# Kernel optimization log

Measured on AMD Instinct MI355X. Metric: run time of the kernel, lower is better.

Reference implementation:

```python
import jax, jax.numpy as jnp
import numpy as np

N = 100000
E = 3200000
IN_DIM, HID_DIM, OUT_DIM = 29, 64, 2


def setup_inputs() -> dict:
    key = jax.random.key(0)
    k1, k2, k3, k4, k5 = jax.random.split(key, 5)
    x = jax.random.normal(k1, (N, IN_DIM), dtype=jnp.float32)
    edge_index = jax.random.randint(k2, (2, E), 0, N, dtype=jnp.int64)
    # GCNConv params: glorot-ish weights, zero bias (bias added after aggregation)
    W1 = jax.random.normal(k3, (IN_DIM, HID_DIM), dtype=jnp.float32) * (1.0 / np.sqrt(IN_DIM))
    b1 = jnp.zeros((HID_DIM,), dtype=jnp.float32)
    W2 = jax.random.normal(k4, (HID_DIM, OUT_DIM), dtype=jnp.float32) * (1.0 / np.sqrt(HID_DIM))
    b2 = jnp.zeros((OUT_DIM,), dtype=jnp.float32)
    return {"x": x, "edge_index": edge_index, "W1": W1, "b1": b1, "W2": W2, "b2": b2}


def _gcn_norm(edge_index, n_nodes):
    # PyG gcn_norm with add_self_loops=True, symmetric D^-1/2 A D^-1/2
    loop = jnp.arange(n_nodes, dtype=edge_index.dtype)
    src = jnp.concatenate([edge_index[0], loop])
    dst = jnp.concatenate([edge_index[1], loop])
    deg = jax.ops.segment_sum(jnp.ones_like(dst, dtype=jnp.float32), dst, num_segments=n_nodes)
    dinv = jnp.where(deg > 0, jax.lax.rsqrt(deg), 0.0)
    norm = dinv[src] * dinv[dst]  # [E + N]
    return src, dst, norm


def _gcn_conv(x, src, dst, norm, W, b):
    h = x @ W                      # [N, d_out] -- transform first (smaller msgs)
    msg = h[src] * norm[:, None]   # [E+N, d_out] gather + scale
    out = jax.ops.segment_sum(msg, dst, num_segments=x.shape[0])  # scatter-add
    return out + b


def reference(x, edge_index, W1, b1, W2, b2):
    src, dst, norm = _gcn_norm(edge_index, x.shape[0])
    h = _gcn_conv(x, src, dst, norm, W1, b1)
    h = jax.nn.relu(h)
    out = _gcn_conv(h, src, dst, norm, W2, b2)
    return out
```

## Files before the change

kernel.cpp:

```cpp
#include <hip/hip_runtime.h>

#define N_NODES 100000
#define N_EDGES 3200000
#define IN_DIM  29
#define HID_DIM 64
#define NBUCK   782
#define BNODES  128
#define CAP     5120
#define EPT     8
#define EPB     4096

#define OFF_CUR   0
#define OFF_ROWS  1024
#define OFF_ROWE  101024
#define OFF_DINV  201024
#define OFF_ZS    301024
#define OFF_EBUF  501024
#define OFF_XS    4504864

static __device__ __forceinline__ unsigned short f2bf(float f) {
    unsigned u = __float_as_uint(f);
    u += 0x7fffu + ((u >> 16) & 1u);
    return (unsigned short)(u >> 16);
}

static __device__ __forceinline__ void unpack_add(float4& acc, uint2 a) {
    acc.x += __uint_as_float(a.x << 16);
    acc.y += __uint_as_float(a.x & 0xFFFF0000u);
    acc.z += __uint_as_float(a.y << 16);
    acc.w += __uint_as_float(a.y & 0xFFFF0000u);
}

__global__ __launch_bounds__(512) void partition_kernel(const int* __restrict__ ei,
        int* __restrict__ gcursor, int* __restrict__ ebuf) {
    __shared__ int lhist[NBUCK];
    __shared__ int lcur[NBUCK];
    int tid = threadIdx.x;
    for (int i = tid; i < NBUCK; i += 512) lhist[i] = 0;
    __syncthreads();

    int base = blockIdx.x * EPB + tid * EPT;
    int dv[EPT], sv[EPT];
    bool valid = (base < N_EDGES);
    if (valid) {
        const int4* dp = (const int4*)(ei + N_EDGES + base);
        const int4* sp = (const int4*)(ei + base);
        #pragma unroll
        for (int q = 0; q < 2; ++q) {
            int4 t = dp[q];
            dv[4*q+0] = t.x; dv[4*q+1] = t.y; dv[4*q+2] = t.z; dv[4*q+3] = t.w;
            int4 u = sp[q];
            sv[4*q+0] = u.x; sv[4*q+1] = u.y; sv[4*q+2] = u.z; sv[4*q+3] = u.w;
        }
        #pragma unroll
        for (int j = 0; j < EPT; ++j) atomicAdd(&lhist[dv[j] >> 7], 1);
    }
    __syncthreads();
    for (int i = tid; i < NBUCK; i += 512) {
        int c = lhist[i];
        lcur[i] = c ? (atomicAdd(&gcursor[i], c) + i * CAP) : 0;
    }
    __syncthreads();
    if (valid) {
        #pragma unroll
        for (int j = 0; j < EPT; ++j) {
            int d = dv[j];
            int pos = atomicAdd(&lcur[d >> 7], 1);
            ebuf[pos] = sv[j] | ((d & 127) << 17);
        }
    }
}

__global__ __launch_bounds__(512) void bucketsort_kernel(const int* __restrict__ gcursor,
        int* __restrict__ ebuf, int* __restrict__ rowStart, int* __restrict__ rowEnd,
        float* __restrict__ dinv, const float* __restrict__ x,
        unsigned int* __restrict__ xsb) {
    __shared__ int   cnt[BNODES];
    __shared__ int   cur[BNODES];
    __shared__ float dls[BNODES];
    __shared__ int   stage[CAP];
    int b = blockIdx.x, tid = threadIdx.x;
    if (tid < BNODES) cnt[tid] = 0;
    __syncthreads();
    int base = b * CAP;
    int size = gcursor[b];

    for (int j = tid; j < size; j += 512)
        atomicAdd(&cnt[((unsigned)ebuf[base + j]) >> 17], 1);
    __syncthreads();

    if (tid < 64) {
        int a = cnt[2 * tid], bb = cnt[2 * tid + 1];
        int s = a + bb;
        int incl = s;
        #pragma unroll
        for (int off = 1; off < 64; off <<= 1) {
            int t = __shfl_up(incl, off);
            if ((int)tid >= off) incl += t;
        }
        int excl = incl - s;
        cur[2 * tid]     = excl;
        cur[2 * tid + 1] = excl + a;
    }
    __syncthreads();

    if (tid < BNODES) {
        int v = cnt[tid];
        int excl = cur[tid];
        int node = b * BNODES + tid;
        if (node < N_NODES) {
            rowStart[node] = base + excl;
            rowEnd[node]   = base + excl + v;
            float dn = rsqrtf((float)v + 1.0f);
            dinv[node] = dn;
            dls[tid] = dn;
        }
    }
    __syncthreads();

    for (int j = tid; j < size; j += 512) {
        unsigned p = (unsigned)ebuf[base + j];
        int pos = atomicAdd(&cur[p >> 17], 1);
        stage[pos] = p & 0x1FFFF;
    }
    __syncthreads();
    for (int j = tid; j < size; j += 512)
        ebuf[base + j] = stage[j];

    for (int i = tid; i < BNODES * 16; i += 512) {
        int dl = i >> 4, kp = i & 15;
        int nd = b * BNODES + dl;
        if (nd < N_NODES) {
            float dn = dls[dl];
            int k0 = kp * 2, k1 = k0 + 1;
            float f0 = (k0 < IN_DIM) ? x[nd * IN_DIM + k0] * dn : 0.0f;
            float f1 = (k1 < IN_DIM) ? x[nd * IN_DIM + k1] * dn : 0.0f;
            unsigned u = (unsigned)f2bf(f0) | ((unsigned)f2bf(f1) << 16);
            xsb[(size_t)nd * 16 + kp] = u;
        }
    }
}

__global__ __launch_bounds__(256) void fused_kernel(const unsigned int* __restrict__ xs_,
        const int* __restrict__ rowStart, const int* __restrict__ rowEnd,
        const int* __restrict__ ebuf, const float* __restrict__ dinv,
        const float* __restrict__ W1, const float* __restrict__ b1,
        const float* __restrict__ W2, float* __restrict__ zs) {
    __shared__ float w1s[IN_DIM * HID_DIM];
    __shared__ float b1s[HID_DIM];
    __shared__ float w2s[HID_DIM * 2];
    int tid = threadIdx.x;
    for (int i = tid; i < IN_DIM * HID_DIM; i += 256) w1s[i] = W1[i];
    if (tid < HID_DIM) {
        b1s[tid] = b1[tid];
        w2s[tid * 2 + 0] = W2[tid * 2 + 0];
        w2s[tid * 2 + 1] = W2[tid * 2 + 1];
    }
    __syncthreads();

    int lane = tid & 63;
    int q = lane >> 3, m = lane & 7;
    const uint2* xsb = (const uint2*)xs_;
    int nodeBase = blockIdx.x * 16 + (tid >> 6) * 4;

    for (int rep = 0; rep < 4; ++rep) {
        int node = nodeBase + rep;
        if (node >= N_NODES) break;

        float4 acc = make_float4(0.f, 0.f, 0.f, 0.f);
        if (q == 0)
            unpack_add(acc, xsb[(size_t)node * 8 + m]);

        int rs = rowStart[node], re = rowEnd[node];
        int last = re - 1;
        for (int j = rs + q; j < re; j += 32) {
            int j1 = j + 8, j2 = j + 16, j3 = j + 24;
            int s0 = ebuf[j];
            int s1 = ebuf[min(j1, last)];
            int s2 = ebuf[min(j2, last)];
            int s3 = ebuf[min(j3, last)];
            uint2 a  = xsb[(size_t)s0 * 8 + m];
            uint2 bb = xsb[(size_t)s1 * 8 + m];
            uint2 c  = xsb[(size_t)s2 * 8 + m];
            uint2 d  = xsb[(size_t)s3 * 8 + m];
            unpack_add(acc, a);
            if (j1 < re) unpack_add(acc, bb);
            if (j2 < re) unpack_add(acc, c);
            if (j3 < re) unpack_add(acc, d);
        }
        #pragma unroll
        for (int msk = 8; msk <= 32; msk <<= 1) {
            acc.x += __shfl_xor(acc.x, msk);
            acc.y += __shfl_xor(acc.y, msk);
            acc.z += __shfl_xor(acc.z, msk);
            acc.w += __shfl_xor(acc.w, msk);
        }
        float dn = dinv[node];
        acc.x *= dn; acc.y *= dn; acc.z *= dn; acc.w *= dn;

        float h = b1s[lane];
        #pragma unroll
        for (int kk = 0; kk < IN_DIM; ++kk) {
            float comp = ((kk & 3) == 0) ? acc.x : ((kk & 3) == 1) ? acc.y
                       : ((kk & 3) == 2) ? acc.z : acc.w;
            h = fmaf(__shfl(comp, kk >> 2), w1s[kk * HID_DIM + lane], h);
        }
        h = fmaxf(h, 0.0f);

        float z0 = h * w2s[lane * 2 + 0];
        float z1 = h * w2s[lane * 2 + 1];
        #pragma unroll
        for (int off = 32; off > 0; off >>= 1) {
            z0 += __shfl_down(z0, off);
            z1 += __shfl_down(z1, off);
        }
        if (lane == 0) {
            zs[node * 2 + 0] = z0 * dn;
            zs[node * 2 + 1] = z1 * dn;
        }
    }
}

__global__ __launch_bounds__(256) void agg2_kernel(const float* __restrict__ zs,
        const int* __restrict__ rowStart, const int* __restrict__ rowEnd,
        const int* __restrict__ ebuf, const float* __restrict__ dinv,
        const float* __restrict__ b2, float* __restrict__ out) {
    int tid = threadIdx.x;
    int node = blockIdx.x * 16 + (tid >> 4);
    if (node >= N_NODES) return;
    int gl = tid & 15;
    const float2* zs2 = (const float2*)zs;
    float a0 = 0.0f, a1 = 0.0f, c0 = 0.0f, c1 = 0.0f;
    int rs = rowStart[node], re = rowEnd[node];
    int last = re - 1;
    for (int j = rs + gl; j < re; j += 32) {
        int j1 = j + 16;
        float2 za = zs2[ebuf[j]];
        float2 zb = zs2[ebuf[min(j1, last)]];
        a0 += za.x; a1 += za.y;
        if (j1 < re) { c0 += zb.x; c1 += zb.y; }
    }
    a0 += c0; a1 += c1;
    a0 += __shfl_xor(a0, 8); a1 += __shfl_xor(a1, 8);
    a0 += __shfl_xor(a0, 4); a1 += __shfl_xor(a1, 4);
    a0 += __shfl_xor(a0, 2); a1 += __shfl_xor(a1, 2);
    a0 += __shfl_xor(a0, 1); a1 += __shfl_xor(a1, 1);
    if (gl == 0) {
        float dn = dinv[node];
        float2 zself = zs2[node];
        float2 o;
        o.x = dn * (a0 + zself.x) + b2[0];
        o.y = dn * (a1 + zself.y) + b2[1];
        ((float2*)out)[node] = o;
    }
}

extern "C" void kernel_launch(void* const* d_in, const int* in_sizes, int n_in,
                              void* d_out, int out_size, void* d_ws, size_t ws_size,
                              hipStream_t stream) {
    const float* x  = (const float*)d_in[0];
    const int*   ei = (const int*)d_in[1];
    const float* W1 = (const float*)d_in[2];
    const float* b1 = (const float*)d_in[3];
    const float* W2 = (const float*)d_in[4];
    const float* b2 = (const float*)d_in[5];
    float* out = (float*)d_out;

    int*   wsi      = (int*)d_ws;
    float* wsf      = (float*)d_ws;
    int*   gcursor  = wsi + OFF_CUR;
    int*   rowStart = wsi + OFF_ROWS;
    int*   rowEnd   = wsi + OFF_ROWE;
    float* dinv     = wsf + OFF_DINV;
    float* zs       = wsf + OFF_ZS;
    int*   ebuf     = wsi + OFF_EBUF;
    unsigned int* xsb = (unsigned int*)(wsi + OFF_XS);

    hipMemsetAsync(gcursor, 0, NBUCK * sizeof(int), stream);
    partition_kernel<<<(N_EDGES + EPB - 1) / EPB, 512, 0, stream>>>(ei, gcursor, ebuf);
    bucketsort_kernel<<<NBUCK, 512, 0, stream>>>(gcursor, ebuf, rowStart, rowEnd, dinv, x, xsb);
    fused_kernel<<<(N_NODES + 15) / 16, 256, 0, stream>>>(xsb, rowStart, rowEnd, ebuf, dinv, W1, b1, W2, zs);
    agg2_kernel<<<(N_NODES + 15) / 16, 256, 0, stream>>>(zs, rowStart, rowEnd, ebuf, dinv, b2, out);
}
```

Before: 229.3 us.

## Split bucket sort into degree count and fuse sort into layer-1 aggregation

Result: slower. 237.9 us (+3.8%).

```diff
diff --git a/kernel.cpp b/kernel.cpp
--- a/kernel.cpp
+++ b/kernel.cpp
@@ -4,19 +4,22 @@
 #define N_EDGES 3200000
 #define IN_DIM  29
 #define HID_DIM 64
-#define NBUCK   782
-#define BNODES  128
-#define CAP     5120
-#define EPT     8
-#define EPB     4096
+#define NBUCK   1563
+#define BNODES  64
+#define CAP     2560
+#define EPT     32
+#define EPB     16384
 
 #define OFF_CUR   0
-#define OFF_ROWS  1024
-#define OFF_ROWE  101024
-#define OFF_DINV  201024
-#define OFF_ZS    301024
-#define OFF_EBUF  501024
-#define OFF_XS    4504864
+#define OFF_DEGC  2048
+#define OFF_DINV  102080
+#define OFF_ROWS  202112
+#define OFF_ROWE  302144
+#define OFF_ZS    402176
+#define OFF_EBUF  602240
+#define OFF_XS    4603520
+
+typedef unsigned uv2 __attribute__((ext_vector_type(2)));
 
 static __device__ __forceinline__ unsigned short f2bf(float f) {
     unsigned u = __float_as_uint(f);
@@ -24,7 +27,7 @@
     return (unsigned short)(u >> 16);
 }
 
-static __device__ __forceinline__ void unpack_add(float4& acc, uint2 a) {
+static __device__ __forceinline__ void unpack_add(float4& acc, uv2 a) {
     acc.x += __uint_as_float(a.x << 16);
     acc.y += __uint_as_float(a.x & 0xFFFF0000u);
     acc.z += __uint_as_float(a.y << 16);
@@ -46,14 +49,14 @@
         const int4* dp = (const int4*)(ei + N_EDGES + base);
         const int4* sp = (const int4*)(ei + base);
         #pragma unroll
-        for (int q = 0; q < 2; ++q) {
+        for (int q = 0; q < 8; ++q) {
             int4 t = dp[q];
             dv[4*q+0] = t.x; dv[4*q+1] = t.y; dv[4*q+2] = t.z; dv[4*q+3] = t.w;
             int4 u = sp[q];
             sv[4*q+0] = u.x; sv[4*q+1] = u.y; sv[4*q+2] = u.z; sv[4*q+3] = u.w;
         }
         #pragma unroll
-        for (int j = 0; j < EPT; ++j) atomicAdd(&lhist[dv[j] >> 7], 1);
+        for (int j = 0; j < EPT; ++j) atomicAdd(&lhist[dv[j] >> 6], 1);
     }
     __syncthreads();
     for (int i = tid; i < NBUCK; i += 512) {
@@ -65,69 +68,37 @@
         #pragma unroll
         for (int j = 0; j < EPT; ++j) {
             int d = dv[j];
-            int pos = atomicAdd(&lcur[d >> 7], 1);
-            ebuf[pos] = sv[j] | ((d & 127) << 17);
-        }
-    }
-}
-
-__global__ __launch_bounds__(512) void bucketsort_kernel(const int* __restrict__ gcursor,
-        int* __restrict__ ebuf, int* __restrict__ rowStart, int* __restrict__ rowEnd,
-        float* __restrict__ dinv, const float* __restrict__ x,
+            int pos = atomicAdd(&lcur[d >> 6], 1);
+            ebuf[pos] = sv[j] | ((d & 63) << 17);
+        }
+    }
+}
+
+__global__ __launch_bounds__(256) void degcnt_kernel(const int* __restrict__ gcursor,
+        const int* __restrict__ ebuf, const float* __restrict__ x,
+        int* __restrict__ degc, float* __restrict__ dinv,
         unsigned int* __restrict__ xsb) {
     __shared__ int   cnt[BNODES];
-    __shared__ int   cur[BNODES];
     __shared__ float dls[BNODES];
-    __shared__ int   stage[CAP];
     int b = blockIdx.x, tid = threadIdx.x;
     if (tid < BNODES) cnt[tid] = 0;
     __syncthreads();
-    int base = b * CAP;
-    int size = gcursor[b];
-
-    for (int j = tid; j < size; j += 512)
+    int base = b * CAP, sz = gcursor[b];
+    for (int j = tid; j < sz; j += 256)
         atomicAdd(&cnt[((unsigned)ebuf[base + j]) >> 17], 1);
     __syncthreads();
-
-    if (tid < 64) {
-        int a = cnt[2 * tid], bb = cnt[2 * tid + 1];
-        int s = a + bb;
-        int incl = s;
-        #pragma unroll
-        for (int off = 1; off < 64; off <<= 1) {
-            int t = __shfl_up(incl, off);
-            if ((int)tid >= off) incl += t;
-        }
-        int excl = incl - s;
-        cur[2 * tid]     = excl;
-        cur[2 * tid + 1] = excl + a;
-    }
-    __syncthreads();
-
     if (tid < BNODES) {
-        int v = cnt[tid];
-        int excl = cur[tid];
         int node = b * BNODES + tid;
         if (node < N_NODES) {
-            rowStart[node] = base + excl;
-            rowEnd[node]   = base + excl + v;
-            float dn = rsqrtf((float)v + 1.0f);
+            int c = cnt[tid];
+            degc[node] = c;
+            float dn = rsqrtf((float)c + 1.0f);
             dinv[node] = dn;
             dls[tid] = dn;
         }
     }
     __syncthreads();
-
-    for (int j = tid; j < size; j += 512) {
-        unsigned p = (unsigned)ebuf[base + j];
-        int pos = atomicAdd(&cur[p >> 17], 1);
-        stage[pos] = p & 0x1FFFF;
-    }
-    __syncthreads();
-    for (int j = tid; j < size; j += 512)
-        ebuf[base + j] = stage[j];
-
-    for (int i = tid; i < BNODES * 16; i += 512) {
+    for (int i = tid; i < BNODES * 16; i += 256) {
         int dl = i >> 4, kp = i & 15;
         int nd = b * BNODES + dl;
         if (nd < N_NODES) {
@@ -135,58 +106,91 @@
             int k0 = kp * 2, k1 = k0 + 1;
             float f0 = (k0 < IN_DIM) ? x[nd * IN_DIM + k0] * dn : 0.0f;
             float f1 = (k1 < IN_DIM) ? x[nd * IN_DIM + k1] * dn : 0.0f;
-            unsigned u = (unsigned)f2bf(f0) | ((unsigned)f2bf(f1) << 16);
-            xsb[(size_t)nd * 16 + kp] = u;
-        }
-    }
-}
-
-__global__ __launch_bounds__(256) void fused_kernel(const unsigned int* __restrict__ xs_,
-        const int* __restrict__ rowStart, const int* __restrict__ rowEnd,
-        const int* __restrict__ ebuf, const float* __restrict__ dinv,
+            xsb[(size_t)nd * 16 + kp] = (unsigned)f2bf(f0) | ((unsigned)f2bf(f1) << 16);
+        }
+    }
+}
+
+__global__ __launch_bounds__(256) void sortfused_kernel(const unsigned int* __restrict__ xs_,
+        const int* __restrict__ gcursor, int* __restrict__ ebuf,
+        const int* __restrict__ degc,
+        int* __restrict__ rowStart, int* __restrict__ rowEnd,
         const float* __restrict__ W1, const float* __restrict__ b1,
         const float* __restrict__ W2, float* __restrict__ zs) {
     __shared__ float w1s[IN_DIM * HID_DIM];
     __shared__ float b1s[HID_DIM];
     __shared__ float w2s[HID_DIM * 2];
-    int tid = threadIdx.x;
+    __shared__ int   cnt[BNODES];
+    __shared__ int   rs_l[BNODES];
+    __shared__ int   cur[BNODES];
+    __shared__ int   stage[CAP];
+    int tid = threadIdx.x, b = blockIdx.x;
     for (int i = tid; i < IN_DIM * HID_DIM; i += 256) w1s[i] = W1[i];
     if (tid < HID_DIM) {
         b1s[tid] = b1[tid];
         w2s[tid * 2 + 0] = W2[tid * 2 + 0];
         w2s[tid * 2 + 1] = W2[tid * 2 + 1];
     }
-    __syncthreads();
-
-    int lane = tid & 63;
+    int base = b * CAP, sz = gcursor[b];
+    if (tid < BNODES) {
+        int node = b * BNODES + tid;
+        cnt[tid] = (node < N_NODES) ? degc[node] : 0;
+    }
+    __syncthreads();
+
+    if (tid < 64) {
+        int c = cnt[tid];
+        int incl = c;
+        #pragma unroll
+        for (int off = 1; off < 64; off <<= 1) {
+            int t = __shfl_up(incl, off);
+            if (tid >= off) incl += t;
+        }
+        int excl = incl - c;
+        rs_l[tid] = excl;
+        cur[tid]  = excl;
+        int node = b * BNODES + tid;
+        if (node < N_NODES) {
+            rowStart[node] = base + excl;
+            rowEnd[node]   = base + excl + c;
+        }
+    }
+    __syncthreads();
+
+    for (int j = tid; j < sz; j += 256) {
+        unsigned p = (unsigned)ebuf[base + j];
+        int pos = atomicAdd(&cur[p >> 17], 1);
+        stage[pos] = p & 0x1FFFF;
+    }
+    __syncthreads();
+    for (int j = tid; j < sz; j += 256)
+        ebuf[base + j] = stage[j];
+
+    int wave = tid >> 6, lane = tid & 63;
     int q = lane >> 3, m = lane & 7;
-    const uint2* xsb = (const uint2*)xs_;
-    int nodeBase = blockIdx.x * 16 + (tid >> 6) * 4;
-
-    for (int rep = 0; rep < 4; ++rep) {
-        int node = nodeBase + rep;
+    const uv2* xsbv = (const uv2*)xs_;
+    for (int dl = wave; dl < BNODES; dl += 4) {
+        int node = b * BNODES + dl;
         if (node >= N_NODES) break;
-
         float4 acc = make_float4(0.f, 0.f, 0.f, 0.f);
         if (q == 0)
-            unpack_add(acc, xsb[(size_t)node * 8 + m]);
-
-        int rs = rowStart[node], re = rowEnd[node];
+            unpack_add(acc, xsbv[(size_t)node * 8 + m]);
+        int rs = rs_l[dl], re = rs + cnt[dl];
         int last = re - 1;
         for (int j = rs + q; j < re; j += 32) {
             int j1 = j + 8, j2 = j + 16, j3 = j + 24;
-            int s0 = ebuf[j];
-            int s1 = ebuf[min(j1, last)];
-            int s2 = ebuf[min(j2, last)];
-            int s3 = ebuf[min(j3, last)];
-            uint2 a  = xsb[(size_t)s0 * 8 + m];
-            uint2 bb = xsb[(size_t)s1 * 8 + m];
-            uint2 c  = xsb[(size_t)s2 * 8 + m];
-            uint2 d  = xsb[(size_t)s3 * 8 + m];
-            unpack_add(acc, a);
-            if (j1 < re) unpack_add(acc, bb);
-            if (j2 < re) unpack_add(acc, c);
-            if (j3 < re) unpack_add(acc, d);
+            int s0 = stage[j];
+            int s1 = stage[min(j1, last)];
+            int s2 = stage[min(j2, last)];
+            int s3 = stage[min(j3, last)];
+            uv2 a0 = xsbv[(size_t)s0 * 8 + m];
+            uv2 a1 = xsbv[(size_t)s1 * 8 + m];
+            uv2 a2 = xsbv[(size_t)s2 * 8 + m];
+            uv2 a3 = xsbv[(size_t)s3 * 8 + m];
+            unpack_add(acc, a0);
+            if (j1 < re) unpack_add(acc, a1);
+            if (j2 < re) unpack_add(acc, a2);
+            if (j3 < re) unpack_add(acc, a3);
         }
         #pragma unroll
         for (int msk = 8; msk <= 32; msk <<= 1) {
@@ -195,7 +199,7 @@
             acc.z += __shfl_xor(acc.z, msk);
             acc.w += __shfl_xor(acc.w, msk);
         }
-        float dn = dinv[node];
+        float dn = rsqrtf((float)cnt[dl] + 1.0f);
         acc.x *= dn; acc.y *= dn; acc.z *= dn; acc.w *= dn;
 
         float h = b1s[lane];
@@ -269,16 +273,18 @@
     int*   wsi      = (int*)d_ws;
     float* wsf      = (float*)d_ws;
     int*   gcursor  = wsi + OFF_CUR;
+    int*   degc     = wsi + OFF_DEGC;
+    float* dinv     = wsf + OFF_DINV;
     int*   rowStart = wsi + OFF_ROWS;
     int*   rowEnd   = wsi + OFF_ROWE;
-    float* dinv     = wsf + OFF_DINV;
     float* zs       = wsf + OFF_ZS;
     int*   ebuf     = wsi + OFF_EBUF;
     unsigned int* xsb = (unsigned int*)(wsi + OFF_XS);
 
     hipMemsetAsync(gcursor, 0, NBUCK * sizeof(int), stream);
     partition_kernel<<<(N_EDGES + EPB - 1) / EPB, 512, 0, stream>>>(ei, gcursor, ebuf);
-    bucketsort_kernel<<<NBUCK, 512, 0, stream>>>(gcursor, ebuf, rowStart, rowEnd, dinv, x, xsb);
-    fused_kernel<<<(N_NODES + 15) / 16, 256, 0, stream>>>(xsb, rowStart, rowEnd, ebuf, dinv, W1, b1, W2, zs);
+    degcnt_kernel<<<NBUCK, 256, 0, stream>>>(gcursor, ebuf, x, degc, dinv, xsb);
+    sortfused_kernel<<<NBUCK, 256, 0, stream>>>(xsb, gcursor, ebuf, degc,
+                                                rowStart, rowEnd, W1, b1, W2, zs);
     agg2_kernel<<<(N_NODES + 15) / 16, 256, 0, stream>>>(zs, rowStart, rowEnd, ebuf, dinv, b2, out);
 }
```
